# Optimization experiments

Measured on AMD Instinct MI355X. Metric: run time of the kernel, lower is better.

Reference implementation:

```python
import jax, jax.numpy as jnp
import numpy as np


def setup_inputs() -> dict:
    key = jax.random.key(0)
    ks = jax.random.split(key, 7)
    n, d_in, d_h = 1024, 1024, 512
    scale = 1.0 / np.sqrt(d_in)
    return {
        "vectors": jax.random.normal(ks[0], (n, d_in), dtype=jnp.float32),
        "W_h": jax.random.normal(ks[1], (d_h, d_in), dtype=jnp.float32) * scale,
        "b_h": jax.random.normal(ks[2], (d_h,), dtype=jnp.float32) * 0.01,
        "W_m": jax.random.normal(ks[3], (d_h, d_in), dtype=jnp.float32) * scale,
        "b_m": jax.random.normal(ks[4], (d_h,), dtype=jnp.float32) * 0.01,
        "w2": jax.random.normal(ks[5], (d_h,), dtype=jnp.float32) * (1.0 / np.sqrt(d_h)),
        "b2": jax.random.normal(ks[6], (1,), dtype=jnp.float32) * 0.01,
    }


def reference(vectors, W_h, b_h, W_m, b_m, w2, b2):
    # Two linear projections: [n, d_h]
    h = vectors @ W_h.T + b_h  # head representations
    m = vectors @ W_m.T + b_m  # modifier representations
    # Pairwise broadcast add: pair[i, j, :] = h[i] + m[j]  -> [n, n, d_h]
    pair = jnp.tanh(h[:, None, :] + m[None, :, :])
    # Linear to scalar + squeeze -> [n, n]
    scores = jnp.einsum("ijh,h->ij", pair, w2) + b2[0]
    return scores
```

## Files before the change

### kernel.cpp

```cpp
#include <hip/hip_runtime.h>
#include <hip/hip_bf16.h>

#define D_IN  1024
#define D_H   512
#define L2E2  2.885390081777927f
#define ECLAMP 15.0f

typedef _Float16 half8 __attribute__((ext_vector_type(8)));
typedef _Float16 half4v __attribute__((ext_vector_type(4)));
typedef float f32x4 __attribute__((ext_vector_type(4)));

__global__ __launch_bounds__(256) void cvt_kernel(
    const float* __restrict__ V,
    const float* __restrict__ Wh, const float* __restrict__ Wm,
    _Float16* __restrict__ Vh, _Float16* __restrict__ Wf)
{
  const int idx = blockIdx.x * 256 + threadIdx.x;
  {
    float4 x = ((const float4*)V)[idx];
    half4v o = { (_Float16)x.x, (_Float16)x.y, (_Float16)x.z, (_Float16)x.w };
    ((half4v*)Vh)[idx] = o;
  }
  {
    const float4* p = (idx < 131072) ? ((const float4*)Wh + idx)
                                     : ((const float4*)Wm + (idx - 131072));
    float4 x = *p;
    half4v o = { (_Float16)x.x, (_Float16)x.y, (_Float16)x.z, (_Float16)x.w };
    ((half4v*)Wf)[idx] = o;
  }
}

__global__ __launch_bounds__(256) void proj_mfma_kernel(
    const _Float16* __restrict__ Vh, const _Float16* __restrict__ Wf,
    const float* __restrict__ bh, const float* __restrict__ bm,
    float* __restrict__ C)
{
  const int tid  = threadIdx.x;
  const int lane = tid & 63;
  const int wid  = tid >> 6;
  const int wi   = wid >> 1, wj = wid & 1;
  const int i0   = (blockIdx.x & 31) * 32;
  const int j0   = (blockIdx.x >> 5) * 64;
  const int r16  = lane & 15;
  const int kg   = lane >> 4;

  const _Float16* A0 = Vh + (size_t)(i0 + 16*wi + r16) * 1024 + kg*8;
  const _Float16* B0 = Wf + (size_t)(j0 + 32*wj + r16) * 1024 + kg*8;
  const _Float16* B1 = B0 + 16 * 1024;

  f32x4 acc0 = {0.f,0.f,0.f,0.f}, acc1 = acc0;
  #pragma unroll 8
  for (int k0 = 0; k0 < D_IN; k0 += 32) {
    half8 a  = *(const half8*)(A0 + k0);
    half8 b0 = *(const half8*)(B0 + k0);
    half8 b1 = *(const half8*)(B1 + k0);
    acc0 = __builtin_amdgcn_mfma_f32_16x16x32_f16(a, b0, acc0, 0, 0, 0);
    acc1 = __builtin_amdgcn_mfma_f32_16x16x32_f16(a, b1, acc1, 0, 0, 0);
  }

  const float* biasp = (j0 < D_H) ? (bh + j0) : (bm + (j0 - D_H));
  #pragma unroll
  for (int fj = 0; fj < 2; ++fj) {
    const f32x4 acc = fj ? acc1 : acc0;
    const int jl = 32*wj + 16*fj + r16;
    const float bias = biasp[jl];
    #pragma unroll
    for (int rr = 0; rr < 4; ++rr) {
      const int il = 16*wi + 4*kg + rr;
      float x = (acc[rr] + bias) * L2E2;
      x = fminf(fmaxf(x, -ECLAMP), ECLAMP);
      C[(size_t)(i0 + il) * 1024 + j0 + jl] = __builtin_amdgcn_exp2f(x);
    }
  }
}

__global__ __launch_bounds__(256) void proj_kernel(
    const float* __restrict__ V,
    const float* __restrict__ Wh, const float* __restrict__ bh,
    const float* __restrict__ Wm, const float* __restrict__ bm,
    float* __restrict__ C)
{
  __shared__ float As[16][68];
  __shared__ float Bs[16][68];

  const int tid = threadIdx.x;
  const int bi  = blockIdx.x & 15;
  const int bj  = blockIdx.x >> 4;
  const int i0  = bi * 64, j0 = bj * 64;
  const int ti  = tid >> 4, tj = tid & 15;
  const int sr  = tid >> 2;
  const int sk  = (tid & 3) << 2;

  const float* Wbase = (j0 < D_H) ? (Wh + (size_t)j0 * D_IN)
                                  : (Wm + (size_t)(j0 - D_H) * D_IN);
  const float* biasp = (j0 < D_H) ? (bh + j0) : (bm + (j0 - D_H));

  const float* arow = V     + (size_t)(i0 + sr) * D_IN + sk;
  const float* brow = Wbase + (size_t)sr        * D_IN + sk;

  float acc[4][4] = {};
  for (int k0 = 0; k0 < D_IN; k0 += 16) {
    float4 av = *(const float4*)(arow + k0);
    float4 bv = *(const float4*)(brow + k0);
    As[sk+0][sr] = av.x; As[sk+1][sr] = av.y; As[sk+2][sr] = av.z; As[sk+3][sr] = av.w;
    Bs[sk+0][sr] = bv.x; Bs[sk+1][sr] = bv.y; Bs[sk+2][sr] = bv.z; Bs[sk+3][sr] = bv.w;
    __syncthreads();
    #pragma unroll
    for (int kk = 0; kk < 16; ++kk) {
      float4 a = *(const float4*)&As[kk][4*ti];
      float4 b = *(const float4*)&Bs[kk][4*tj];
      #pragma unroll
      for (int x = 0; x < 4; ++x)
        #pragma unroll
        for (int y = 0; y < 4; ++y)
          acc[x][y] = fmaf((&a.x)[x], (&b.x)[y], acc[x][y]);
    }
    __syncthreads();
  }

  const int jl = 4 * tj;
  #pragma unroll
  for (int aa = 0; aa < 4; ++aa) {
    const int i = i0 + 4*ti + aa;
    float4 o;
    #pragma unroll
    for (int bb = 0; bb < 4; ++bb) {
      float x = (acc[aa][bb] + biasp[jl+bb]) * L2E2;
      x = fminf(fmaxf(x, -ECLAMP), ECLAMP);
      (&o.x)[bb] = __builtin_amdgcn_exp2f(x);
    }
    *(float4*)(C + (size_t)i * 1024 + j0 + jl) = o;
  }
}

__global__ __launch_bounds__(256) void score_kernel(
    const float* __restrict__ C,
    const float* __restrict__ w2,
    const float* __restrict__ b2,
    float* __restrict__ out)
{
  __shared__ float hs[2][32][34];
  __shared__ float ms[2][32][34];
  __shared__ float wred[4];

  const int tid = threadIdx.x;
  const int bi  = blockIdx.x & 31;
  const int bj  = blockIdx.x >> 5;
  const int i0  = bi * 32, j0 = bj * 32;
  const int ti  = tid >> 4, tj = tid & 15;
  const int sr  = tid >> 3;
  const int sk  = (tid & 7) << 2;

  float sw = 0.f;
  for (int t = tid; t < D_H; t += 256) sw += w2[t];
  #pragma unroll
  for (int off = 32; off > 0; off >>= 1) sw += __shfl_down(sw, off, 64);
  if ((tid & 63) == 0) wred[tid >> 6] = sw;

  const float* hrow = C + (size_t)(i0 + sr) * 1024 + sk;
  const float* mrow = C + (size_t)(j0 + sr) * 1024 + D_H + sk;

  float4 hv = *(const float4*)(hrow);
  float4 mv = *(const float4*)(mrow);

  float a00 = 0.f, a01 = 0.f, a10 = 0.f, a11 = 0.f;
  int p = 0;

  for (int k0 = 0; k0 < D_H; k0 += 32) {
    ((float2*)&hs[p][sr][sk])[0] = make_float2(hv.x, hv.y);
    ((float2*)&hs[p][sr][sk+2])[0] = make_float2(hv.z, hv.w);
    ((float2*)&ms[p][sr][sk])[0] = make_float2(mv.x, mv.y);
    ((float2*)&ms[p][sr][sk+2])[0] = make_float2(mv.z, mv.w);
    __syncthreads();

    if (k0 + 32 < D_H) {
      hv = *(const float4*)(hrow + k0 + 32);
      mv = *(const float4*)(mrow + k0 + 32);
    }

    #pragma unroll
    for (int g = 0; g < 8; ++g) {
      const int kk = 4 * g;
      const float wA = w2[k0 + kk + 0];
      const float wB = w2[k0 + kk + 1];
      const float wC = w2[k0 + kk + 2];
      const float wD = w2[k0 + kk + 3];
      float4 eh0 = *(const float4*)&hs[p][2*ti    ][kk];
      float4 eh1 = *(const float4*)&hs[p][2*ti + 1][kk];
      float4 em0 = *(const float4*)&ms[p][2*tj    ][kk];
      float4 em1 = *(const float4*)&ms[p][2*tj + 1][kk];

      #define TERM(EH, EM, ACC)                                        \
      {                                                                \
        float uA = fmaf((EH).x, (EM).x, 1.f);                          \
        float uB = fmaf((EH).y, (EM).y, 1.f);                          \
        float uC = fmaf((EH).z, (EM).z, 1.f);                          \
        float uD = fmaf((EH).w, (EM).w, 1.f);                          \
        float dAB = uA * uB, dCD = uC * uD;                            \
        float nAB = fmaf(wB, uA, wA * uB);                             \
        float nCD = fmaf(wD, uC, wC * uD);                             \
        float den = dAB * dCD;                                         \
        float num = fmaf(nCD, dAB, nAB * dCD);                         \
        ACC = fmaf(num, __builtin_amdgcn_rcpf(den), ACC);              \
      }
      TERM(eh0, em0, a00)
      TERM(eh0, em1, a01)
      TERM(eh1, em0, a10)
      TERM(eh1, em1, a11)
      #undef TERM
    }
    p ^= 1;
  }

  const float base = b2[0] + wred[0] + wred[1] + wred[2] + wred[3];
  const int i = i0 + 2*ti, j = j0 + 2*tj;
  float2 r0, r1;
  r0.x = fmaf(-2.f, a00, base); r0.y = fmaf(-2.f, a01, base);
  r1.x = fmaf(-2.f, a10, base); r1.y = fmaf(-2.f, a11, base);
  *(float2*)(out + (size_t)i       * 1024 + j) = r0;
  *(float2*)(out + (size_t)(i + 1) * 1024 + j) = r1;
}

extern "C" void kernel_launch(void* const* d_in, const int* in_sizes, int n_in,
                              void* d_out, int out_size, void* d_ws, size_t ws_size,
                              hipStream_t stream) {
  const float* V  = (const float*)d_in[0];
  const float* Wh = (const float*)d_in[1];
  const float* bh = (const float*)d_in[2];
  const float* Wm = (const float*)d_in[3];
  const float* bm = (const float*)d_in[4];
  const float* w2 = (const float*)d_in[5];
  const float* b2 = (const float*)d_in[6];
  float* outp = (float*)d_out;

  char* ws = (char*)d_ws;
  float* C = (float*)ws;
  if (ws_size >= (size_t)(8u << 20)) {
    _Float16* Vh = (_Float16*)(ws + (4u << 20));
    _Float16* Wf = (_Float16*)(ws + (6u << 20));
    cvt_kernel<<<dim3(1024), dim3(256), 0, stream>>>(V, Wh, Wm, Vh, Wf);
    proj_mfma_kernel<<<dim3(512), dim3(256), 0, stream>>>(Vh, Wf, bh, bm, C);
  } else {
    proj_kernel<<<dim3(256), dim3(256), 0, stream>>>(V, Wh, bh, Wm, bm, C);
  }
  score_kernel<<<dim3(1024), dim3(256), 0, stream>>>(C, w2, b2, outp);
}
```

Before: 87.74 us.

## Retile projection MFMA to 64x64 blocks and stride score-kernel thread mapping

The projection kernel now uses 512-thread blocks covering 64x64 output tiles, with each wave computing two row fragments against one weight fragment. Blocks are swizzled so that neighbouring blocks share input rows in cache. The score kernel changes its thread-to-output mapping from contiguous 2x2 pairs to rows and columns strided by 16, which changes shared-memory access patterns to reduce bank conflicts. It also gains a min-blocks launch hint. The strided layout makes output stores scalar rather than float2, and the launch hints may raise register pressure.

```diff
diff --git a/kernel.cpp b/kernel.cpp
--- a/kernel.cpp
+++ b/kernel.cpp
@@ -30,7 +30,7 @@
   }
 }
 
-__global__ __launch_bounds__(256) void proj_mfma_kernel(
+__global__ __launch_bounds__(512, 2) void proj_mfma_kernel(
     const _Float16* __restrict__ Vh, const _Float16* __restrict__ Wf,
     const float* __restrict__ bh, const float* __restrict__ bm,
     float* __restrict__ C)
@@ -38,35 +38,37 @@
   const int tid  = threadIdx.x;
   const int lane = tid & 63;
   const int wid  = tid >> 6;
-  const int wi   = wid >> 1, wj = wid & 1;
-  const int i0   = (blockIdx.x & 31) * 32;
-  const int j0   = (blockIdx.x >> 5) * 64;
+  const int wi   = wid >> 2, wj = wid & 3;
+  const int bid  = blockIdx.x;
+  const int swz  = (bid & 7) * 32 + (bid >> 3);
+  const int i0   = (swz & 15) * 64;
+  const int j0   = (swz >> 4) * 64;
   const int r16  = lane & 15;
   const int kg   = lane >> 4;
 
-  const _Float16* A0 = Vh + (size_t)(i0 + 16*wi + r16) * 1024 + kg*8;
-  const _Float16* B0 = Wf + (size_t)(j0 + 32*wj + r16) * 1024 + kg*8;
-  const _Float16* B1 = B0 + 16 * 1024;
+  const _Float16* A0 = Vh + (size_t)(i0 + 32*wi + r16) * 1024 + kg*8;
+  const _Float16* A1 = A0 + 16 * 1024;
+  const _Float16* B0 = Wf + (size_t)(j0 + 16*wj + r16) * 1024 + kg*8;
 
   f32x4 acc0 = {0.f,0.f,0.f,0.f}, acc1 = acc0;
   #pragma unroll 8
   for (int k0 = 0; k0 < D_IN; k0 += 32) {
-    half8 a  = *(const half8*)(A0 + k0);
+    half8 a0 = *(const half8*)(A0 + k0);
+    half8 a1 = *(const half8*)(A1 + k0);
     half8 b0 = *(const half8*)(B0 + k0);
-    half8 b1 = *(const half8*)(B1 + k0);
-    acc0 = __builtin_amdgcn_mfma_f32_16x16x32_f16(a, b0, acc0, 0, 0, 0);
-    acc1 = __builtin_amdgcn_mfma_f32_16x16x32_f16(a, b1, acc1, 0, 0, 0);
+    acc0 = __builtin_amdgcn_mfma_f32_16x16x32_f16(a0, b0, acc0, 0, 0, 0);
+    acc1 = __builtin_amdgcn_mfma_f32_16x16x32_f16(a1, b0, acc1, 0, 0, 0);
   }
 
   const float* biasp = (j0 < D_H) ? (bh + j0) : (bm + (j0 - D_H));
-  #pragma unroll
-  for (int fj = 0; fj < 2; ++fj) {
-    const f32x4 acc = fj ? acc1 : acc0;
-    const int jl = 32*wj + 16*fj + r16;
-    const float bias = biasp[jl];
+  const int jl = 16*wj + r16;
+  const float bias = biasp[jl];
+  #pragma unroll
+  for (int fi = 0; fi < 2; ++fi) {
+    const f32x4 acc = fi ? acc1 : acc0;
     #pragma unroll
     for (int rr = 0; rr < 4; ++rr) {
-      const int il = 16*wi + 4*kg + rr;
+      const int il = 32*wi + 16*fi + 4*kg + rr;
       float x = (acc[rr] + bias) * L2E2;
       x = fminf(fmaxf(x, -ECLAMP), ECLAMP);
       C[(size_t)(i0 + il) * 1024 + j0 + jl] = __builtin_amdgcn_exp2f(x);
@@ -84,9 +86,7 @@
   __shared__ float Bs[16][68];
 
   const int tid = threadIdx.x;
-  const int bi  = blockIdx.x & 15;
-  const int bj  = blockIdx.x >> 4;
-  const int i0  = bi * 64, j0 = bj * 64;
+  const int i0  = (blockIdx.x & 15) * 64, j0 = (blockIdx.x >> 4) * 64;
   const int ti  = tid >> 4, tj = tid & 15;
   const int sr  = tid >> 2;
   const int sk  = (tid & 3) << 2;
@@ -133,7 +133,7 @@
   }
 }
 
-__global__ __launch_bounds__(256) void score_kernel(
+__global__ __launch_bounds__(256, 4) void score_kernel(
     const float* __restrict__ C,
     const float* __restrict__ w2,
     const float* __restrict__ b2,
@@ -148,6 +148,7 @@
   const int bj  = blockIdx.x >> 5;
   const int i0  = bi * 32, j0 = bj * 32;
   const int ti  = tid >> 4, tj = tid & 15;
+
   const int sr  = tid >> 3;
   const int sk  = (tid & 7) << 2;
 
@@ -163,14 +164,14 @@
   float4 hv = *(const float4*)(hrow);
   float4 mv = *(const float4*)(mrow);
 
-  float a00 = 0.f, a01 = 0.f, a10 = 0.f, a11 = 0.f;
+  float acc[2][2] = {};
   int p = 0;
 
   for (int k0 = 0; k0 < D_H; k0 += 32) {
-    ((float2*)&hs[p][sr][sk])[0] = make_float2(hv.x, hv.y);
-    ((float2*)&hs[p][sr][sk+2])[0] = make_float2(hv.z, hv.w);
-    ((float2*)&ms[p][sr][sk])[0] = make_float2(mv.x, mv.y);
-    ((float2*)&ms[p][sr][sk+2])[0] = make_float2(mv.z, mv.w);
+    *(float2*)&hs[p][sr][sk]     = make_float2(hv.x, hv.y);
+    *(float2*)&hs[p][sr][sk + 2] = make_float2(hv.z, hv.w);
+    *(float2*)&ms[p][sr][sk]     = make_float2(mv.x, mv.y);
+    *(float2*)&ms[p][sr][sk + 2] = make_float2(mv.z, mv.w);
     __syncthreads();
 
     if (k0 + 32 < D_H) {
@@ -185,40 +186,46 @@
       const float wB = w2[k0 + kk + 1];
       const float wC = w2[k0 + kk + 2];
       const float wD = w2[k0 + kk + 3];
-      float4 eh0 = *(const float4*)&hs[p][2*ti    ][kk];
-      float4 eh1 = *(const float4*)&hs[p][2*ti + 1][kk];
-      float4 em0 = *(const float4*)&ms[p][2*tj    ][kk];
-      float4 em1 = *(const float4*)&ms[p][2*tj + 1][kk];
-
-      #define TERM(EH, EM, ACC)                                        \
-      {                                                                \
-        float uA = fmaf((EH).x, (EM).x, 1.f);                          \
-        float uB = fmaf((EH).y, (EM).y, 1.f);                          \
-        float uC = fmaf((EH).z, (EM).z, 1.f);                          \
-        float uD = fmaf((EH).w, (EM).w, 1.f);                          \
-        float dAB = uA * uB, dCD = uC * uD;                            \
-        float nAB = fmaf(wB, uA, wA * uB);                             \
-        float nCD = fmaf(wD, uC, wC * uD);                             \
-        float den = dAB * dCD;                                         \
-        float num = fmaf(nCD, dAB, nAB * dCD);                         \
-        ACC = fmaf(num, __builtin_amdgcn_rcpf(den), ACC);              \
+      float2 em_[2][2], eh_[2][2];
+      #pragma unroll
+      for (int c = 0; c < 2; ++c) {
+        em_[c][0] = *(const float2*)&ms[p][tj + 16*c][kk];
+        em_[c][1] = *(const float2*)&ms[p][tj + 16*c][kk + 2];
       }
-      TERM(eh0, em0, a00)
-      TERM(eh0, em1, a01)
-      TERM(eh1, em0, a10)
-      TERM(eh1, em1, a11)
-      #undef TERM
+      #pragma unroll
+      for (int a = 0; a < 2; ++a) {
+        eh_[a][0] = *(const float2*)&hs[p][ti + 16*a][kk];
+        eh_[a][1] = *(const float2*)&hs[p][ti + 16*a][kk + 2];
+      }
+      #pragma unroll
+      for (int a = 0; a < 2; ++a)
+        #pragma unroll
+        for (int c = 0; c < 2; ++c) {
+          float uA = fmaf(eh_[a][0].x, em_[c][0].x, 1.f);
+          float uB = fmaf(eh_[a][0].y, em_[c][0].y, 1.f);
+          float uC = fmaf(eh_[a][1].x, em_[c][1].x, 1.f);
+          float uD = fmaf(eh_[a][1].y, em_[c][1].y, 1.f);
+          float dAB = uA * uB, dCD = uC * uD;
+          float nAB = fmaf(wB, uA, wA * uB);
+          float nCD = fmaf(wD, uC, wC * uD);
+          float den = dAB * dCD;
+          float num = fmaf(nCD, dAB, nAB * dCD);
+          acc[a][c] = fmaf(num, __builtin_amdgcn_rcpf(den), acc[a][c]);
+        }
     }
     p ^= 1;
   }
 
   const float base = b2[0] + wred[0] + wred[1] + wred[2] + wred[3];
-  const int i = i0 + 2*ti, j = j0 + 2*tj;
-  float2 r0, r1;
-  r0.x = fmaf(-2.f, a00, base); r0.y = fmaf(-2.f, a01, base);
-  r1.x = fmaf(-2.f, a10, base); r1.y = fmaf(-2.f, a11, base);
-  *(float2*)(out + (size_t)i       * 1024 + j) = r0;
-  *(float2*)(out + (size_t)(i + 1) * 1024 + j) = r1;
+  #pragma unroll
+  for (int a = 0; a < 2; ++a) {
+    const int i = i0 + ti + 16*a;
+    #pragma unroll
+    for (int c = 0; c < 2; ++c) {
+      const int j = j0 + tj + 16*c;
+      out[(size_t)i * 1024 + j] = fmaf(-2.f, acc[a][c], base);
+    }
+  }
 }
 
 extern "C" void kernel_launch(void* const* d_in, const int* in_sizes, int n_in,
@@ -235,11 +242,12 @@
 
   char* ws = (char*)d_ws;
   float* C = (float*)ws;
+
   if (ws_size >= (size_t)(8u << 20)) {
     _Float16* Vh = (_Float16*)(ws + (4u << 20));
     _Float16* Wf = (_Float16*)(ws + (6u << 20));
     cvt_kernel<<<dim3(1024), dim3(256), 0, stream>>>(V, Wh, Wm, Vh, Wf);
-    proj_mfma_kernel<<<dim3(512), dim3(256), 0, stream>>>(Vh, Wf, bh, bm, C);
+    proj_mfma_kernel<<<dim3(256), dim3(512), 0, stream>>>(Vh, Wf, bh, bm, C);
   } else {
     proj_kernel<<<dim3(256), dim3(256), 0, stream>>>(V, Wh, bh, Wm, bm, C);
   }
```

New measurement: 89.06 us. About the same (+1.5%).
